# Performance work log

Measured on AMD Instinct MI355X. Metric: run time of the kernel, lower is better.

Reference implementation:

```python
import jax, jax.numpy as jnp
import numpy as np

B, N, D = 1024, 100, 768  # N=100 is hard-coded by th_embedding Linear(100,1)
EPS_LN, EPS = 1e-5, 1e-8


def setup_inputs() -> dict:
    key = jax.random.key(0)
    k0, k1, k2 = jax.random.split(key, 3)
    return {
        "x": jax.random.normal(k0, (B, N, D), dtype=jnp.float32),
        "cluster_center": jax.random.normal(k1, (B, 1, D), dtype=jnp.float32),
        "alpha": jnp.ones((1,), dtype=jnp.float32),
        "ln_gamma": jnp.ones((D,), dtype=jnp.float32),
        "ln_beta": jnp.zeros((D,), dtype=jnp.float32),
        "th_w": jax.random.normal(k2, (1, N), dtype=jnp.float32) * 0.1,
        "th_b": jnp.zeros((1,), dtype=jnp.float32),
    }


def reference(x, cluster_center, alpha, ln_gamma, ln_beta, th_w, th_b):
    # LayerNorm over last dim
    mu = jnp.mean(x, axis=-1, keepdims=True)
    var = jnp.mean((x - mu) ** 2, axis=-1, keepdims=True)
    xn = (x - mu) / jnp.sqrt(var + EPS_LN) * ln_gamma + ln_beta  # [B,N,D]

    # pairwise cosine similarity  [B,N,N]
    num = jnp.einsum("bnd,bmd->bnm", xn, xn)
    nrm = jnp.linalg.norm(xn, axis=-1, keepdims=True)            # [B,N,1]
    den = nrm * jnp.swapaxes(nrm, -2, -1)                        # [B,N,N]
    cos_sim = num / (den + EPS)

    # density + min-max normalize  [B,N]
    density = jnp.sum(cos_sim, axis=-1)
    d_max = jnp.max(density, axis=-1, keepdims=True)
    d_min = jnp.min(density, axis=-1, keepdims=True)
    density = (density - d_min) / (d_max - d_min + EPS)

    # learned threshold: Flatten -> Linear(100,1) -> Sigmoid, scaled by alpha
    th = jax.nn.sigmoid(density @ th_w.T + th_b) * alpha         # [B,1]

    # ReLU gate + normalize
    density = jax.nn.relu(density - th)
    density_th = density / (jnp.sum(density, axis=1, keepdims=True) + EPS)

    # weighted shift of cluster center
    distance_map = xn - cluster_center                           # [B,N,D] (broadcast of repeat)
    shift = distance_map * density_th[:, :, None]
    shift_avg = jnp.mean(shift, axis=1, keepdims=True)           # [B,1,D]
    return cluster_center + shift_avg
```

## Files before the change

kernel.cpp:

```cpp
#include <hip/hip_runtime.h>
#include <math.h>

#define BT     1024
#define NROW   100
#define DDIM   768
#define EPS_LN 1e-5f
#define EPSF   1e-8f

#define LDS_BYTES 160144

__device__ __forceinline__ float bflo(unsigned int p) {
    union { unsigned int u; float f; } c; c.u = p << 16; return c.f;
}
__device__ __forceinline__ float bfhi(unsigned int p) {
    union { unsigned int u; float f; } c; c.u = p & 0xFFFF0000u; return c.f;
}
__device__ __forceinline__ unsigned int cvtpk(float lo, float hi) {
    unsigned int r;
    asm("v_cvt_pk_bf16_f32 %0, %1, %2" : "=v"(r) : "v"(lo), "v"(hi));
    return r;
}
__device__ __forceinline__ float wave_sum(float v) {
#pragma unroll
    for (int m = 32; m >= 1; m >>= 1) v += __shfl_xor(v, m, 64);
    return v;
}
__device__ __forceinline__ float half_sum(float v) {
#pragma unroll
    for (int m = 16; m >= 1; m >>= 1) v += __shfl_xor(v, m, 64);
    return v;
}

extern "C" __global__ void __launch_bounds__(BT, 4)
ccs_kernel(const float* __restrict__ x,
           const float* __restrict__ cc,
           const float* __restrict__ alpha,
           const float* __restrict__ gamma,
           const float* __restrict__ beta,
           const float* __restrict__ thw,
           const float* __restrict__ thb,
           float* __restrict__ out)
{
    extern __shared__ char lds[];
    unsigned int* u = (unsigned int*)lds;
    float* gammaL = (float*)(lds + 153600);
    float* betaL  = (float*)(lds + 156672);
    float* S      = (float*)(lds + 153600);
    float* dens   = (float*)(lds + 156672);
    float* w2     = (float*)(lds + 157072);
    float* Wsh    = (float*)(lds + 157472);
    float* nrm    = (float*)(lds + 159744);

    const int tid = threadIdx.x;
    const int w   = tid >> 6;
    const int l   = tid & 63;
    const int li  = l & 31;
    const int hw  = (w << 1) | (l >> 5);
    const int b   = blockIdx.x;
    const float* xb = x + (size_t)b * (NROW * DDIM);

    float thwa = 0.f, thwb = 0.f, alphav = 0.f, thbv = 0.f;
    if (w == 0) {
        thwa = thw[l];
        if (l < NROW - 64) thwb = thw[64 + l];
        alphav = alpha[0];
        thbv   = thb[0];
    }
    float2 ccv = make_float2(0.f, 0.f);
    if (tid < 384) ccv = *(const float2*)(cc + (size_t)b * DDIM + 2 * tid);

    const int base  = 4 * li;
    const int pcnt  = (hw < 4) ? 4 : 3;
    float xf[24];
    {
        const float* xr = xb + hw * DDIM + base;
#pragma unroll
        for (int k = 0; k < 6; ++k)
            *(float4*)&xf[4 * k] = *(const float4*)(xr + 128 * k);
    }

    if (tid < DDIM) { gammaL[tid] = gamma[tid]; betaL[tid] = beta[tid]; }
    __syncthreads();

#pragma unroll
    for (int r = 0; r < 4; ++r) {
        if (r >= pcnt) break;
        const int row = hw + 32 * r;

        float p0 = 0.f, p1 = 0.f;
#pragma unroll
        for (int m = 0; m < 24; ++m) { p0 += xf[m]; p1 += xf[m] * xf[m]; }

        float xn1[24];
        if (r + 1 < pcnt) {
            const float* xr = xb + (row + 32) * DDIM + base;
#pragma unroll
            for (int k = 0; k < 6; ++k)
                *(float4*)&xn1[4 * k] = *(const float4*)(xr + 128 * k);
        }

#pragma unroll
        for (int m = 16; m >= 1; m >>= 1) {
            p0 += __shfl_xor(p0, m, 64);
            p1 += __shfl_xor(p1, m, 64);
        }
        const float mu  = p0 * (1.0f / DDIM);
        const float var = p1 * (1.0f / DDIM) - mu * mu;
        const float A   = rsqrtf(var + EPS_LN);
        const float nmuA = -mu * A;

        float q = 0.f;
#pragma unroll
        for (int k = 0; k < 6; ++k) {
            const float4 g4 = *(const float4*)&gammaL[base + 128 * k];
            const float4 b4 = *(const float4*)&betaL [base + 128 * k];
            const float* gp = (const float*)&g4;
            const float* bp = (const float*)&b4;
#pragma unroll
            for (int i = 0; i < 4; ++i) {
                const float t = fmaf(xf[4 * k + i], A, nmuA);
                const float v = fmaf(t, gp[i], bp[i]);
                xf[4 * k + i] = v;
                q += v * v;
            }
        }
        q = half_sum(q);
        const float qc  = fmaxf(q, 1e-30f);
        const float inv = rsqrtf(qc);
        const float nr  = qc * inv;

        unsigned int* ur = u + row * 384 + 2 * li;
#pragma unroll
        for (int k = 0; k < 6; ++k) {
            uint2 pk;
            pk.x = cvtpk(xf[4 * k + 0] * inv, xf[4 * k + 1] * inv);
            pk.y = cvtpk(xf[4 * k + 2] * inv, xf[4 * k + 3] * inv);
            *(uint2*)&ur[64 * k] = pk;
        }
        if (li == 0) nrm[row] = nr;

        if (r + 1 < pcnt) {
#pragma unroll
            for (int m = 0; m < 24; ++m) xf[m] = xn1[m];
        }
    }
    __syncthreads();

    if (tid < 384) {
        float ax = 0.f, ay = 0.f;
        const unsigned int* up = u + tid;
#pragma unroll 4
        for (int n = 0; n < NROW; ++n) {
            const unsigned int pw = up[n * 384];
            ax += bflo(pw); ay += bfhi(pw);
        }
        *(float2*)&S[2 * tid] = make_float2(ax, ay);
    }
    __syncthreads();

    const int cnt = (w < 4) ? 7 : 6;
    float Sv[12];
#pragma unroll
    for (int k = 0; k < 3; ++k)
        *(float4*)&Sv[4 * k] = *(const float4*)&S[k * 256 + 4 * l];

    float dot[7];
#pragma unroll
    for (int r = 0; r < 7; ++r) dot[r] = 0.f;
#pragma unroll
    for (int r = 0; r < 7; ++r) {
        if (r < cnt) {
            const unsigned int* ur = u + (w + 16 * r) * 384;
            float d = 0.f;
#pragma unroll
            for (int k = 0; k < 3; ++k) {
                const uint2 p = *(const uint2*)&ur[k * 128 + 2 * l];
                d += bflo(p.x) * Sv[4*k+0] + bfhi(p.x) * Sv[4*k+1]
                   + bflo(p.y) * Sv[4*k+2] + bfhi(p.y) * Sv[4*k+3];
            }
            dot[r] = d;
        }
    }
#pragma unroll
    for (int msk = 32; msk >= 1; msk >>= 1) {
#pragma unroll
        for (int r = 0; r < 7; ++r) dot[r] += __shfl_xor(dot[r], msk, 64);
    }
    if (l == 0) {
#pragma unroll
        for (int r = 0; r < 7; ++r)
            if (r < cnt) dens[w + 16 * r] = dot[r];
    }
    __syncthreads();

    if (w == 0) {
        const float va = dens[l];
        const bool  hb = (l < NROW - 64);
        const float vb = hb ? dens[64 + l] : 0.f;

        float mxv = hb ? fmaxf(va, vb) : va;
        float mnv = hb ? fminf(va, vb) : va;
#pragma unroll
        for (int m = 32; m >= 1; m >>= 1) {
            mxv = fmaxf(mxv, __shfl_xor(mxv, m, 64));
            mnv = fminf(mnv, __shfl_xor(mnv, m, 64));
        }
        const float rng = 1.0f / (mxv - mnv + EPSF);
        const float ra  = (va - mnv) * rng;
        const float rb  = (vb - mnv) * rng;

        float td = ra * thwa + (hb ? rb * thwb : 0.f);
        td = wave_sum(td);
        const float z  = td + thbv;
        const float th = alphav / (1.0f + expf(-z));

        const float ga  = fmaxf(ra - th, 0.f);
        const float gb_ = hb ? fmaxf(rb - th, 0.f) : 0.f;
        const float sg  = wave_sum(ga + gb_);
        const float wf  = 1.0f / (sg + EPSF);

        w2[l] = ga * wf * nrm[l];
        if (hb) w2[64 + l] = gb_ * wf * nrm[64 + l];
        if (l == 0) Wsh[0] = sg * wf;
    }
    __syncthreads();

    if (tid < 384) {
        float ax = 0.f, ay = 0.f;
        const unsigned int* up = u + tid;
#pragma unroll 4
        for (int n = 0; n < NROW; ++n) {
            const float wv = w2[n];
            const unsigned int pw = up[n * 384];
            ax += wv * bflo(pw); ay += wv * bfhi(pw);
        }
        const float W = Wsh[0];
        float2 o;
        o.x = ccv.x + (ax - ccv.x * W) * (1.0f / NROW);
        o.y = ccv.y + (ay - ccv.y * W) * (1.0f / NROW);
        *(float2*)(out + (size_t)b * DDIM + 2 * tid) = o;
    }
}

extern "C" void kernel_launch(void* const* d_in, const int* in_sizes, int n_in,
                              void* d_out, int out_size, void* d_ws, size_t ws_size,
                              hipStream_t stream) {
    const float* x     = (const float*)d_in[0];
    const float* cc    = (const float*)d_in[1];
    const float* alpha = (const float*)d_in[2];
    const float* gamma = (const float*)d_in[3];
    const float* beta  = (const float*)d_in[4];
    const float* thw   = (const float*)d_in[5];
    const float* thb   = (const float*)d_in[6];
    float* out = (float*)d_out;

    ccs_kernel<<<1024, BT, LDS_BYTES, stream>>>(x, cc, alpha, gamma, beta, thw, thb, out);
}
```

Baseline: 88.47 us.

## Make blocks persistent over four batch items with cross-item prefetch

Launches 256 blocks that each loop over four batch items instead of one block per item, prefetching the first rows of the next item while the current item's density and weighted-sum phases run. This is meant to hide global load latency and block launch and tail cost between waves. Gamma and beta are stored packed as bf16 in LDS, and barriers use explicit waitcnt+s_barrier. The bf16 gamma/beta add rounding error, and per-block serialization removes the inter-block overlap the hardware scheduler previously provided.

```diff
diff --git a/kernel.cpp b/kernel.cpp
--- a/kernel.cpp
+++ b/kernel.cpp
@@ -2,12 +2,16 @@
 #include <math.h>
 
 #define BT     1024
+#define GRID   256
+#define NITEMS 4
 #define NROW   100
 #define DDIM   768
 #define EPS_LN 1e-5f
 #define EPSF   1e-8f
 
-#define LDS_BYTES 160144
+#define LDS_BYTES 160948
+
+#define BARRIER() asm volatile("s_waitcnt lgkmcnt(0)\n\ts_barrier" ::: "memory")
 
 __device__ __forceinline__ float bflo(unsigned int p) {
     union { unsigned int u; float f; } c; c.u = p << 16; return c.f;
@@ -42,14 +46,13 @@
            float* __restrict__ out)
 {
     extern __shared__ char lds[];
-    unsigned int* u = (unsigned int*)lds;
-    float* gammaL = (float*)(lds + 153600);
-    float* betaL  = (float*)(lds + 156672);
-    float* S      = (float*)(lds + 153600);
-    float* dens   = (float*)(lds + 156672);
-    float* w2     = (float*)(lds + 157072);
-    float* Wsh    = (float*)(lds + 157472);
-    float* nrm    = (float*)(lds + 159744);
+    unsigned int* u   = (unsigned int*)lds;
+    float*        S   = (float*)(lds + 153600);
+    unsigned int* gbL = (unsigned int*)(lds + 156672);
+    float*        nrm = (float*)(lds + 159744);
+    float*        dens= (float*)(lds + 160144);
+    float*        w2  = (float*)(lds + 160544);
+    float*        Wsh = (float*)(lds + 160944);
 
     const int tid = threadIdx.x;
     const int w   = tid >> 6;
@@ -57,7 +60,6 @@
     const int li  = l & 31;
     const int hw  = (w << 1) | (l >> 5);
     const int b   = blockIdx.x;
-    const float* xb = x + (size_t)b * (NROW * DDIM);
 
     float thwa = 0.f, thwb = 0.f, alphav = 0.f, thbv = 0.f;
     if (w == 0) {
@@ -66,179 +68,197 @@
         alphav = alpha[0];
         thbv   = thb[0];
     }
-    float2 ccv = make_float2(0.f, 0.f);
-    if (tid < 384) ccv = *(const float2*)(cc + (size_t)b * DDIM + 2 * tid);
-
-    const int base  = 4 * li;
-    const int pcnt  = (hw < 4) ? 4 : 3;
+
+    const int base = 4 * li;
+    const int pcnt = (hw < 4) ? 4 : 3;
+    const int cnt  = (w  < 4) ? 7 : 6;
+
     float xf[24];
     {
-        const float* xr = xb + hw * DDIM + base;
+        const float* xr = x + (size_t)b * (NROW * DDIM) + hw * DDIM + base;
 #pragma unroll
         for (int k = 0; k < 6; ++k)
             *(float4*)&xf[4 * k] = *(const float4*)(xr + 128 * k);
     }
 
-    if (tid < DDIM) { gammaL[tid] = gamma[tid]; betaL[tid] = beta[tid]; }
-    __syncthreads();
-
-#pragma unroll
-    for (int r = 0; r < 4; ++r) {
-        if (r >= pcnt) break;
-        const int row = hw + 32 * r;
-
-        float p0 = 0.f, p1 = 0.f;
-#pragma unroll
-        for (int m = 0; m < 24; ++m) { p0 += xf[m]; p1 += xf[m] * xf[m]; }
-
-        float xn1[24];
-        if (r + 1 < pcnt) {
-            const float* xr = xb + (row + 32) * DDIM + base;
+    if (tid < 384) {
+        const float2 g2 = *(const float2*)(gamma + 2 * tid);
+        const float2 b2 = *(const float2*)(beta  + 2 * tid);
+        gbL[tid]       = cvtpk(g2.x, g2.y);
+        gbL[384 + tid] = cvtpk(b2.x, b2.y);
+    }
+    BARRIER();
+
+    for (int it = 0; it < NITEMS; ++it) {
+        const int bi = b + GRID * it;
+        const float* xb = x + (size_t)bi * (NROW * DDIM);
+
+#pragma unroll
+        for (int r = 0; r < 4; ++r) {
+            if (r >= pcnt) break;
+            const int row = hw + 32 * r;
+
+            float p0 = 0.f, p1 = 0.f;
+#pragma unroll
+            for (int m = 0; m < 24; ++m) { p0 += xf[m]; p1 += xf[m] * xf[m]; }
+
+            float xn1[24];
+            if (r + 1 < pcnt) {
+                const float* xr = xb + (row + 32) * DDIM + base;
+#pragma unroll
+                for (int k = 0; k < 6; ++k)
+                    *(float4*)&xn1[4 * k] = *(const float4*)(xr + 128 * k);
+            }
+
+#pragma unroll
+            for (int m = 16; m >= 1; m >>= 1) {
+                p0 += __shfl_xor(p0, m, 64);
+                p1 += __shfl_xor(p1, m, 64);
+            }
+            const float mu   = p0 * (1.0f / DDIM);
+            const float var  = p1 * (1.0f / DDIM) - mu * mu;
+            const float A    = rsqrtf(var + EPS_LN);
+            const float nmuA = -mu * A;
+
+            float q = 0.f;
+#pragma unroll
+            for (int k = 0; k < 6; ++k) {
+                const uint2 gw = *(const uint2*)&gbL[64 * k + 2 * li];
+                const uint2 bw = *(const uint2*)&gbL[384 + 64 * k + 2 * li];
+                const float g0 = bflo(gw.x), g1 = bfhi(gw.x), g2 = bflo(gw.y), g3 = bfhi(gw.y);
+                const float b0 = bflo(bw.x), b1 = bfhi(bw.x), b2 = bflo(bw.y), b3 = bfhi(bw.y);
+                float t, v;
+                t = fmaf(xf[4*k+0], A, nmuA); v = fmaf(t, g0, b0); xf[4*k+0] = v; q += v * v;
+                t = fmaf(xf[4*k+1], A, nmuA); v = fmaf(t, g1, b1); xf[4*k+1] = v; q += v * v;
+                t = fmaf(xf[4*k+2], A, nmuA); v = fmaf(t, g2, b2); xf[4*k+2] = v; q += v * v;
+                t = fmaf(xf[4*k+3], A, nmuA); v = fmaf(t, g3, b3); xf[4*k+3] = v; q += v * v;
+            }
+            q = half_sum(q);
+            const float qc  = fmaxf(q, 1e-30f);
+            const float inv = rsqrtf(qc);
+            const float nr  = qc * inv;
+
+            unsigned int* ur = u + row * 384 + 2 * li;
+#pragma unroll
+            for (int k = 0; k < 6; ++k) {
+                uint2 pk;
+                pk.x = cvtpk(xf[4 * k + 0] * inv, xf[4 * k + 1] * inv);
+                pk.y = cvtpk(xf[4 * k + 2] * inv, xf[4 * k + 3] * inv);
+                *(uint2*)&ur[64 * k] = pk;
+            }
+            if (li == 0) nrm[row] = nr;
+
+            if (r + 1 < pcnt) {
+#pragma unroll
+                for (int m = 0; m < 24; ++m) xf[m] = xn1[m];
+            }
+        }
+
+        if (it + 1 < NITEMS) {
+            const float* xr = x + (size_t)(bi + GRID) * (NROW * DDIM) + hw * DDIM + base;
 #pragma unroll
             for (int k = 0; k < 6; ++k)
-                *(float4*)&xn1[4 * k] = *(const float4*)(xr + 128 * k);
-        }
-
-#pragma unroll
-        for (int m = 16; m >= 1; m >>= 1) {
-            p0 += __shfl_xor(p0, m, 64);
-            p1 += __shfl_xor(p1, m, 64);
-        }
-        const float mu  = p0 * (1.0f / DDIM);
-        const float var = p1 * (1.0f / DDIM) - mu * mu;
-        const float A   = rsqrtf(var + EPS_LN);
-        const float nmuA = -mu * A;
-
-        float q = 0.f;
-#pragma unroll
-        for (int k = 0; k < 6; ++k) {
-            const float4 g4 = *(const float4*)&gammaL[base + 128 * k];
-            const float4 b4 = *(const float4*)&betaL [base + 128 * k];
-            const float* gp = (const float*)&g4;
-            const float* bp = (const float*)&b4;
-#pragma unroll
-            for (int i = 0; i < 4; ++i) {
-                const float t = fmaf(xf[4 * k + i], A, nmuA);
-                const float v = fmaf(t, gp[i], bp[i]);
-                xf[4 * k + i] = v;
-                q += v * v;
-            }
-        }
-        q = half_sum(q);
-        const float qc  = fmaxf(q, 1e-30f);
-        const float inv = rsqrtf(qc);
-        const float nr  = qc * inv;
-
-        unsigned int* ur = u + row * 384 + 2 * li;
-#pragma unroll
-        for (int k = 0; k < 6; ++k) {
-            uint2 pk;
-            pk.x = cvtpk(xf[4 * k + 0] * inv, xf[4 * k + 1] * inv);
-            pk.y = cvtpk(xf[4 * k + 2] * inv, xf[4 * k + 3] * inv);
-            *(uint2*)&ur[64 * k] = pk;
-        }
-        if (li == 0) nrm[row] = nr;
-
-        if (r + 1 < pcnt) {
-#pragma unroll
-            for (int m = 0; m < 24; ++m) xf[m] = xn1[m];
-        }
-    }
-    __syncthreads();
-
-    if (tid < 384) {
-        float ax = 0.f, ay = 0.f;
-        const unsigned int* up = u + tid;
+                *(float4*)&xf[4 * k] = *(const float4*)(xr + 128 * k);
+        }
+        BARRIER();
+
+        if (tid < 384) {
+            float ax = 0.f, ay = 0.f;
+            const unsigned int* up = u + tid;
 #pragma unroll 4
-        for (int n = 0; n < NROW; ++n) {
-            const unsigned int pw = up[n * 384];
-            ax += bflo(pw); ay += bfhi(pw);
-        }
-        *(float2*)&S[2 * tid] = make_float2(ax, ay);
-    }
-    __syncthreads();
-
-    const int cnt = (w < 4) ? 7 : 6;
-    float Sv[12];
-#pragma unroll
-    for (int k = 0; k < 3; ++k)
-        *(float4*)&Sv[4 * k] = *(const float4*)&S[k * 256 + 4 * l];
-
-    float dot[7];
-#pragma unroll
-    for (int r = 0; r < 7; ++r) dot[r] = 0.f;
-#pragma unroll
-    for (int r = 0; r < 7; ++r) {
-        if (r < cnt) {
-            const unsigned int* ur = u + (w + 16 * r) * 384;
-            float d = 0.f;
-#pragma unroll
-            for (int k = 0; k < 3; ++k) {
-                const uint2 p = *(const uint2*)&ur[k * 128 + 2 * l];
-                d += bflo(p.x) * Sv[4*k+0] + bfhi(p.x) * Sv[4*k+1]
-                   + bflo(p.y) * Sv[4*k+2] + bfhi(p.y) * Sv[4*k+3];
-            }
-            dot[r] = d;
-        }
-    }
-#pragma unroll
-    for (int msk = 32; msk >= 1; msk >>= 1) {
-#pragma unroll
-        for (int r = 0; r < 7; ++r) dot[r] += __shfl_xor(dot[r], msk, 64);
-    }
-    if (l == 0) {
-#pragma unroll
-        for (int r = 0; r < 7; ++r)
-            if (r < cnt) dens[w + 16 * r] = dot[r];
-    }
-    __syncthreads();
-
-    if (w == 0) {
-        const float va = dens[l];
-        const bool  hb = (l < NROW - 64);
-        const float vb = hb ? dens[64 + l] : 0.f;
-
-        float mxv = hb ? fmaxf(va, vb) : va;
-        float mnv = hb ? fminf(va, vb) : va;
-#pragma unroll
-        for (int m = 32; m >= 1; m >>= 1) {
-            mxv = fmaxf(mxv, __shfl_xor(mxv, m, 64));
-            mnv = fminf(mnv, __shfl_xor(mnv, m, 64));
-        }
-        const float rng = 1.0f / (mxv - mnv + EPSF);
-        const float ra  = (va - mnv) * rng;
-        const float rb  = (vb - mnv) * rng;
-
-        float td = ra * thwa + (hb ? rb * thwb : 0.f);
-        td = wave_sum(td);
-        const float z  = td + thbv;
-        const float th = alphav / (1.0f + expf(-z));
-
-        const float ga  = fmaxf(ra - th, 0.f);
-        const float gb_ = hb ? fmaxf(rb - th, 0.f) : 0.f;
-        const float sg  = wave_sum(ga + gb_);
-        const float wf  = 1.0f / (sg + EPSF);
-
-        w2[l] = ga * wf * nrm[l];
-        if (hb) w2[64 + l] = gb_ * wf * nrm[64 + l];
-        if (l == 0) Wsh[0] = sg * wf;
-    }
-    __syncthreads();
-
-    if (tid < 384) {
-        float ax = 0.f, ay = 0.f;
-        const unsigned int* up = u + tid;
+            for (int n = 0; n < NROW; ++n) {
+                const unsigned int pw = up[n * 384];
+                ax += bflo(pw); ay += bfhi(pw);
+            }
+            *(float2*)&S[2 * tid] = make_float2(ax, ay);
+        }
+        BARRIER();
+
+        float Sv[12];
+#pragma unroll
+        for (int k = 0; k < 3; ++k)
+            *(float4*)&Sv[4 * k] = *(const float4*)&S[k * 256 + 4 * l];
+
+        float dot[7];
+#pragma unroll
+        for (int r = 0; r < 7; ++r) dot[r] = 0.f;
+#pragma unroll
+        for (int r = 0; r < 7; ++r) {
+            if (r < cnt) {
+                const unsigned int* ur = u + (w + 16 * r) * 384;
+                float d = 0.f;
+#pragma unroll
+                for (int k = 0; k < 3; ++k) {
+                    const uint2 p = *(const uint2*)&ur[k * 128 + 2 * l];
+                    d += bflo(p.x) * Sv[4*k+0] + bfhi(p.x) * Sv[4*k+1]
+                       + bflo(p.y) * Sv[4*k+2] + bfhi(p.y) * Sv[4*k+3];
+                }
+                dot[r] = d;
+            }
+        }
+#pragma unroll
+        for (int msk = 32; msk >= 1; msk >>= 1) {
+#pragma unroll
+            for (int r = 0; r < 7; ++r) dot[r] += __shfl_xor(dot[r], msk, 64);
+        }
+        if (l == 0) {
+#pragma unroll
+            for (int r = 0; r < 7; ++r)
+                if (r < cnt) dens[w + 16 * r] = dot[r];
+        }
+        BARRIER();
+
+        float2 ccv = make_float2(0.f, 0.f);
+        if (tid < 384) ccv = *(const float2*)(cc + (size_t)bi * DDIM + 2 * tid);
+
+        if (w == 0) {
+            const float va = dens[l];
+            const bool  hb = (l < NROW - 64);
+            const float vb = hb ? dens[64 + l] : 0.f;
+
+            float mxv = hb ? fmaxf(va, vb) : va;
+            float mnv = hb ? fminf(va, vb) : va;
+#pragma unroll
+            for (int m = 32; m >= 1; m >>= 1) {
+                mxv = fmaxf(mxv, __shfl_xor(mxv, m, 64));
+                mnv = fminf(mnv, __shfl_xor(mnv, m, 64));
+            }
+            const float rng = 1.0f / (mxv - mnv + EPSF);
+            const float ra  = (va - mnv) * rng;
+            const float rb  = (vb - mnv) * rng;
+
+            float td = ra * thwa + (hb ? rb * thwb : 0.f);
+            td = wave_sum(td);
+            const float z  = td + thbv;
+            const float th = alphav / (1.0f + expf(-z));
+
+            const float ga  = fmaxf(ra - th, 0.f);
+            const float gb_ = hb ? fmaxf(rb - th, 0.f) : 0.f;
+            const float sg  = wave_sum(ga + gb_);
+            const float wf  = 1.0f / (sg + EPSF);
+
+            w2[l] = ga * wf * nrm[l];
+            if (hb) w2[64 + l] = gb_ * wf * nrm[64 + l];
+            if (l == 0) Wsh[0] = sg * wf;
+        }
+        BARRIER();
+
+        if (tid < 384) {
+            float ax = 0.f, ay = 0.f;
+            const unsigned int* up = u + tid;
 #pragma unroll 4
-        for (int n = 0; n < NROW; ++n) {
-            const float wv = w2[n];
-            const unsigned int pw = up[n * 384];
-            ax += wv * bflo(pw); ay += wv * bfhi(pw);
-        }
-        const float W = Wsh[0];
-        float2 o;
-        o.x = ccv.x + (ax - ccv.x * W) * (1.0f / NROW);
-        o.y = ccv.y + (ay - ccv.y * W) * (1.0f / NROW);
-        *(float2*)(out + (size_t)b * DDIM + 2 * tid) = o;
+            for (int n = 0; n < NROW; ++n) {
+                const float wv = w2[n];
+                const unsigned int pw = up[n * 384];
+                ax += wv * bflo(pw); ay += wv * bfhi(pw);
+            }
+            const float W = Wsh[0];
+            float2 o;
+            o.x = ccv.x + (ax - ccv.x * W) * (1.0f / NROW);
+            o.y = ccv.y + (ay - ccv.y * W) * (1.0f / NROW);
+            *(float2*)(out + (size_t)bi * DDIM + 2 * tid) = o;
+        }
+        BARRIER();
     }
 }
 
@@ -254,5 +274,5 @@
     const float* thb   = (const float*)d_in[6];
     float* out = (float*)d_out;
 
-    ccs_kernel<<<1024, BT, LDS_BYTES, stream>>>(x, cc, alpha, gamma, beta, thw, thb, out);
-}
+    ccs_kernel<<<GRID, BT, LDS_BYTES, stream>>>(x, cc, alpha, gamma, beta, thw, thb, out);
+}
```

Result: slower. 94.83 us (+7.2%).

## Use DPP reductions, register-held gamma/beta, and half-wave density dot products

Applied to the files above, without the earlier changes.

Gamma and beta are now loaded straight into registers as packed bf16, which removes their LDS staging and one block-wide barrier. Cross-lane reductions in LayerNorm switch from shuffles to DPP row shifts plus a ds_swizzle broadcast. The density stage now reuses the LayerNorm row-to-half-wave mapping with 128-bit LDS reads, replacing seven full-wave butterfly reductions per wave. The risks are extra register pressure from the packed gamma/beta arrays (including an unused gpk/bpk block) and bf16 rounding of gamma/beta.

```diff
diff --git a/kernel.cpp b/kernel.cpp
--- a/kernel.cpp
+++ b/kernel.cpp
@@ -7,7 +7,7 @@
 #define EPS_LN 1e-5f
 #define EPSF   1e-8f
 
-#define LDS_BYTES 160144
+#define LDS_BYTES 157876
 
 __device__ __forceinline__ float bflo(unsigned int p) {
     union { unsigned int u; float f; } c; c.u = p << 16; return c.f;
@@ -25,10 +25,21 @@
     for (int m = 32; m >= 1; m >>= 1) v += __shfl_xor(v, m, 64);
     return v;
 }
-__device__ __forceinline__ float half_sum(float v) {
-#pragma unroll
-    for (int m = 16; m >= 1; m >>= 1) v += __shfl_xor(v, m, 64);
+
+#define DPPADD(v, ctrl) \
+    v += __int_as_float(__builtin_amdgcn_update_dpp(0, __float_as_int(v), ctrl, 0xf, 0xf, true))
+
+__device__ __forceinline__ float dpp_half_sum(float v) {
+    DPPADD(v, 0x111);
+    DPPADD(v, 0x112);
+    DPPADD(v, 0x114);
+    DPPADD(v, 0x118);
+    DPPADD(v, 0x142);
     return v;
+}
+__device__ __forceinline__ float dpp_half_sum_bcast(float v) {
+    v = dpp_half_sum(v);
+    return __int_as_float(__builtin_amdgcn_ds_swizzle(__float_as_int(v), 0x03E0));
 }
 
 extern "C" __global__ void __launch_bounds__(BT, 4)
@@ -42,14 +53,12 @@
            float* __restrict__ out)
 {
     extern __shared__ char lds[];
-    unsigned int* u = (unsigned int*)lds;
-    float* gammaL = (float*)(lds + 153600);
-    float* betaL  = (float*)(lds + 156672);
-    float* S      = (float*)(lds + 153600);
-    float* dens   = (float*)(lds + 156672);
-    float* w2     = (float*)(lds + 157072);
-    float* Wsh    = (float*)(lds + 157472);
-    float* nrm    = (float*)(lds + 159744);
+    unsigned int* u   = (unsigned int*)lds;
+    float* S    = (float*)(lds + 153600);
+    float* nrm  = (float*)(lds + 156672);
+    float* dens = (float*)(lds + 157072);
+    float* w2   = (float*)(lds + 157472);
+    float* Wsh  = (float*)(lds + 157872);
 
     const int tid = threadIdx.x;
     const int w   = tid >> 6;
@@ -59,6 +68,17 @@
     const int b   = blockIdx.x;
     const float* xb = x + (size_t)b * (NROW * DDIM);
 
+    const int base = 4 * li;
+    const int pcnt = (hw < 4) ? 4 : 3;
+
+    float xf[24];
+    {
+        const float* xr = xb + hw * DDIM + base;
+#pragma unroll
+        for (int k = 0; k < 6; ++k)
+            *(float4*)&xf[4 * k] = *(const float4*)(xr + 128 * k);
+    }
+
     float thwa = 0.f, thwb = 0.f, alphav = 0.f, thbv = 0.f;
     if (w == 0) {
         thwa = thw[l];
@@ -69,18 +89,25 @@
     float2 ccv = make_float2(0.f, 0.f);
     if (tid < 384) ccv = *(const float2*)(cc + (size_t)b * DDIM + 2 * tid);
 
-    const int base  = 4 * li;
-    const int pcnt  = (hw < 4) ? 4 : 3;
-    float xf[24];
-    {
-        const float* xr = xb + hw * DDIM + base;
-#pragma unroll
-        for (int k = 0; k < 6; ++k)
-            *(float4*)&xf[4 * k] = *(const float4*)(xr + 128 * k);
-    }
-
-    if (tid < DDIM) { gammaL[tid] = gamma[tid]; betaL[tid] = beta[tid]; }
-    __syncthreads();
+    uint2 gpk[3], bpk[3];
+#pragma unroll
+    for (int k = 0; k < 3; ++k) {
+        const float4 g4 = *(const float4*)(gamma + 256 * k + base);
+        const float4 g5 = *(const float4*)(gamma + 256 * k + 128 + base);
+        const float4 b4 = *(const float4*)(beta  + 256 * k + base);
+        const float4 b5 = *(const float4*)(beta  + 256 * k + 128 + base);
+        gpk[k].x = cvtpk(g4.x, g4.y); gpk[k].y = cvtpk(g4.z, g4.w);
+        bpk[k].x = cvtpk(b4.x, b4.y); bpk[k].y = cvtpk(b4.z, b4.w);
+        (void)g5; (void)b5;
+    }
+    uint2 gp6[6], bp6[6];
+#pragma unroll
+    for (int k = 0; k < 6; ++k) {
+        const float4 g4 = *(const float4*)(gamma + 128 * k + base);
+        const float4 b4 = *(const float4*)(beta  + 128 * k + base);
+        gp6[k].x = cvtpk(g4.x, g4.y); gp6[k].y = cvtpk(g4.z, g4.w);
+        bp6[k].x = cvtpk(b4.x, b4.y); bp6[k].y = cvtpk(b4.z, b4.w);
+    }
 
 #pragma unroll
     for (int r = 0; r < 4; ++r) {
@@ -89,7 +116,7 @@
 
         float p0 = 0.f, p1 = 0.f;
 #pragma unroll
-        for (int m = 0; m < 24; ++m) { p0 += xf[m]; p1 += xf[m] * xf[m]; }
+        for (int m = 0; m < 24; ++m) { p0 += xf[m]; p1 = fmaf(xf[m], xf[m], p1); }
 
         float xn1[24];
         if (r + 1 < pcnt) {
@@ -99,32 +126,27 @@
                 *(float4*)&xn1[4 * k] = *(const float4*)(xr + 128 * k);
         }
 
-#pragma unroll
-        for (int m = 16; m >= 1; m >>= 1) {
-            p0 += __shfl_xor(p0, m, 64);
-            p1 += __shfl_xor(p1, m, 64);
-        }
-        const float mu  = p0 * (1.0f / DDIM);
-        const float var = p1 * (1.0f / DDIM) - mu * mu;
-        const float A   = rsqrtf(var + EPS_LN);
+        p0 = dpp_half_sum_bcast(p0);
+        p1 = dpp_half_sum_bcast(p1);
+        const float mu   = p0 * (1.0f / DDIM);
+        const float var  = p1 * (1.0f / DDIM) - mu * mu;
+        const float A    = rsqrtf(var + EPS_LN);
         const float nmuA = -mu * A;
 
         float q = 0.f;
 #pragma unroll
         for (int k = 0; k < 6; ++k) {
-            const float4 g4 = *(const float4*)&gammaL[base + 128 * k];
-            const float4 b4 = *(const float4*)&betaL [base + 128 * k];
-            const float* gp = (const float*)&g4;
-            const float* bp = (const float*)&b4;
-#pragma unroll
-            for (int i = 0; i < 4; ++i) {
-                const float t = fmaf(xf[4 * k + i], A, nmuA);
-                const float v = fmaf(t, gp[i], bp[i]);
-                xf[4 * k + i] = v;
-                q += v * v;
-            }
-        }
-        q = half_sum(q);
+            const float g0 = bflo(gp6[k].x), g1 = bfhi(gp6[k].x);
+            const float g2 = bflo(gp6[k].y), g3 = bfhi(gp6[k].y);
+            const float b0 = bflo(bp6[k].x), b1 = bfhi(bp6[k].x);
+            const float b2 = bflo(bp6[k].y), b3 = bfhi(bp6[k].y);
+            float t, v;
+            t = fmaf(xf[4*k+0], A, nmuA); v = fmaf(t, g0, b0); xf[4*k+0] = v; q = fmaf(v, v, q);
+            t = fmaf(xf[4*k+1], A, nmuA); v = fmaf(t, g1, b1); xf[4*k+1] = v; q = fmaf(v, v, q);
+            t = fmaf(xf[4*k+2], A, nmuA); v = fmaf(t, g2, b2); xf[4*k+2] = v; q = fmaf(v, v, q);
+            t = fmaf(xf[4*k+3], A, nmuA); v = fmaf(t, g3, b3); xf[4*k+3] = v; q = fmaf(v, v, q);
+        }
+        q = dpp_half_sum_bcast(q);
         const float qc  = fmaxf(q, 1e-30f);
         const float inv = rsqrtf(qc);
         const float nr  = qc * inv;
@@ -158,38 +180,30 @@
     }
     __syncthreads();
 
-    const int cnt = (w < 4) ? 7 : 6;
-    float Sv[12];
-#pragma unroll
-    for (int k = 0; k < 3; ++k)
-        *(float4*)&Sv[4 * k] = *(const float4*)&S[k * 256 + 4 * l];
-
-    float dot[7];
-#pragma unroll
-    for (int r = 0; r < 7; ++r) dot[r] = 0.f;
-#pragma unroll
-    for (int r = 0; r < 7; ++r) {
-        if (r < cnt) {
-            const unsigned int* ur = u + (w + 16 * r) * 384;
+    {
+        float Sv[24];
+#pragma unroll
+        for (int k = 0; k < 3; ++k) {
+            *(float4*)&Sv[8 * k]     = *(const float4*)&S[256 * k + 8 * li];
+            *(float4*)&Sv[8 * k + 4] = *(const float4*)&S[256 * k + 8 * li + 4];
+        }
+#pragma unroll
+        for (int r = 0; r < 4; ++r) {
+            if (r >= pcnt) break;
+            const int row = hw + 32 * r;
+            const unsigned int* ur = u + row * 384 + 4 * li;
             float d = 0.f;
 #pragma unroll
             for (int k = 0; k < 3; ++k) {
-                const uint2 p = *(const uint2*)&ur[k * 128 + 2 * l];
-                d += bflo(p.x) * Sv[4*k+0] + bfhi(p.x) * Sv[4*k+1]
-                   + bflo(p.y) * Sv[4*k+2] + bfhi(p.y) * Sv[4*k+3];
+                const uint4 pw = *(const uint4*)&ur[128 * k];
+                d = fmaf(bflo(pw.x), Sv[8*k+0], d); d = fmaf(bfhi(pw.x), Sv[8*k+1], d);
+                d = fmaf(bflo(pw.y), Sv[8*k+2], d); d = fmaf(bfhi(pw.y), Sv[8*k+3], d);
+                d = fmaf(bflo(pw.z), Sv[8*k+4], d); d = fmaf(bfhi(pw.z), Sv[8*k+5], d);
+                d = fmaf(bflo(pw.w), Sv[8*k+6], d); d = fmaf(bfhi(pw.w), Sv[8*k+7], d);
             }
-            dot[r] = d;
-        }
-    }
-#pragma unroll
-    for (int msk = 32; msk >= 1; msk >>= 1) {
-#pragma unroll
-        for (int r = 0; r < 7; ++r) dot[r] += __shfl_xor(dot[r], msk, 64);
-    }
-    if (l == 0) {
-#pragma unroll
-        for (int r = 0; r < 7; ++r)
-            if (r < cnt) dens[w + 16 * r] = dot[r];
+            d = dpp_half_sum(d);
+            if (li == 31) dens[row] = d;
+        }
     }
     __syncthreads();
 
@@ -232,7 +246,7 @@
         for (int n = 0; n < NROW; ++n) {
             const float wv = w2[n];
             const unsigned int pw = up[n * 384];
-            ax += wv * bflo(pw); ay += wv * bfhi(pw);
+            ax = fmaf(wv, bflo(pw), ax); ay = fmaf(wv, bfhi(pw), ay);
         }
         const float W = Wsh[0];
         float2 o;
```

After: 81.19 us. 1.09x faster.
